# Kernel tuning notes

Hardware: AMD Instinct MI355X
Metric: run time of the kernel (lower is better)

## Reference

```python
import jax, jax.numpy as jnp
import numpy as np

B, L, C, A = 32, 50, 80, 3
IMG = 480.0
STRIDES = (8, 16, 32)
OBJ_SCALE, NOOBJ_SCALE, CLS_SCALE, COORD_SCALE = 5.0, 1.0, 1.0, 1.0
IOU_IGNORE = 0.6


def setup_inputs() -> dict:
    key = jax.random.key(0)
    ks = jax.random.split(key, 8)
    anchors = jnp.array([[0.05, 0.07], [0.12, 0.15], [0.25, 0.30]], jnp.float32)
    preds0 = jax.random.normal(ks[0], (B, 60, 60, A * (5 + C)), jnp.float32)
    preds1 = jax.random.normal(ks[1], (B, 30, 30, A * (5 + C)), jnp.float32)
    preds2 = jax.random.normal(ks[2], (B, 15, 15, A * (5 + C)), jnp.float32)
    cls = jax.random.randint(ks[3], (B, L, 1), 0, C).astype(jnp.float32)
    xy = jax.random.uniform(ks[4], (B, L, 2), minval=0.2, maxval=0.8)
    wh = jax.random.uniform(ks[5], (B, L, 2), minval=0.05, maxval=0.3)
    valid = (jax.random.uniform(ks[6], (B, L, 1)) < 0.6).astype(jnp.float32)
    # gt_labels in loss layout: [cx, cy, w, h, class], padded boxes have w=h=0
    gt_labels = jnp.concatenate([xy, wh * valid, cls], -1)
    return {"preds0": preds0, "preds1": preds1, "preds2": preds2,
            "gt_labels": gt_labels, "anchors": anchors}


def get_detector_mask(gt, anchors_l, H, W):
    # gt: [B,L,5] (cx,cy,w,h,class) normalized; anchors_l in grid units
    Bv, Lv, _ = gt.shape
    Av = anchors_l.shape[0]
    scale = jnp.array([W, H, W, H], jnp.float32)
    box = gt[..., :4] * scale                                  # grid units
    valid = box[..., 2] > 0.0                                  # [B,L]
    j = jnp.clip(jnp.floor(box[..., 0]), 0, W - 1).astype(jnp.int32)
    i = jnp.clip(jnp.floor(box[..., 1]), 0, H - 1).astype(jnp.int32)
    wh = box[..., 2:4]                                         # [B,L,2]
    inter = jnp.prod(jnp.minimum(wh[:, :, None, :], anchors_l[None, None]), -1)
    iou = inter / (jnp.prod(wh, -1)[..., None]
                   + jnp.prod(anchors_l, -1)[None, None] - inter + 1e-9)
    k = jnp.argmax(iou, -1)                                    # best anchor [B,L]
    b = jnp.arange(Bv, dtype=jnp.int32)[:, None]
    N = Bv * H * W * Av
    flat = ((b * H + i) * W + j) * Av + k
    flat = jnp.where(valid, flat, N)                           # invalid -> sentinel
    mask = jnp.zeros(N + 1, jnp.float32).at[flat.reshape(-1)].set(1.0)[:N]
    mask = mask.reshape(Bv, H, W, Av, 1)
    anc = anchors_l[k]                                         # [B,L,2]
    safe_wh = jnp.where(valid[..., None], wh, 1.0)
    adj = jnp.concatenate([
        (box[..., 0] - j.astype(jnp.float32))[..., None],
        (box[..., 1] - i.astype(jnp.float32))[..., None],
        jnp.log(safe_wh / anc),
        gt[..., 4:5]], -1)                                     # [B,L,5]
    mtb = jnp.zeros((N + 1, 5), jnp.float32).at[flat.reshape(-1)].set(
        adj.reshape(-1, 5))[:N].reshape(Bv, H, W, Av, 5)
    return mask, mtb


def yolo_head(feats, anchors_l):
    Bv, H, W, _ = feats.shape
    Av = anchors_l.shape[0]
    f = feats.reshape(Bv, H, W, Av, 5 + C)
    gy, gx = jnp.meshgrid(jnp.arange(H, dtype=jnp.float32),
                          jnp.arange(W, dtype=jnp.float32), indexing='ij')
    grid = jnp.stack([gx, gy], -1)[None, :, :, None, :]        # [1,H,W,1,2]
    conv = jnp.array([W, H], jnp.float32)
    box_xy = jax.nn.sigmoid(f[..., :2])
    box_wh = jnp.exp(f[..., 2:4])
    pred_xy = (box_xy + grid) / conv                           # normalized
    pred_wh = box_wh * anchors_l / conv
    return f, box_xy, pred_xy, pred_wh


def level_loss(f, box_xy, pred_xy, pred_wh, gt, mask, mtb):
    # IoU of every predicted box against every GT box -> ignore mask
    pmin = (pred_xy - pred_wh * 0.5)[..., None, :]             # [B,H,W,A,1,2]
    pmax = (pred_xy + pred_wh * 0.5)[..., None, :]
    tmin = (gt[..., :2] - gt[..., 2:4] * 0.5)[:, None, None, None]  # [B,1,1,1,L,2]
    tmax = (gt[..., :2] + gt[..., 2:4] * 0.5)[:, None, None, None]
    wh_i = jnp.clip(jnp.minimum(pmax, tmax) - jnp.maximum(pmin, tmin), 0.0)
    inter = jnp.prod(wh_i, -1)                                 # [B,H,W,A,L]
    parea = jnp.prod(pred_wh, -1)[..., None]
    tarea = jnp.prod(gt[..., 2:4], -1)[:, None, None, None]
    iou = inter / (parea + tarea - inter + 1e-9)
    best = jnp.max(iou, -1, keepdims=True)                     # [B,H,W,A,1]
    obj_det = (best > IOU_IGNORE).astype(f.dtype)
    pred_conf = jax.nn.sigmoid(f[..., 4:5])
    no_obj_loss = NOOBJ_SCALE * (1.0 - obj_det) * (1.0 - mask) * pred_conf ** 2
    obj_loss = OBJ_SCALE * mask * (1.0 - pred_conf) ** 2
    pred_class = jax.nn.softmax(f[..., 5:], -1)
    onehot = jax.nn.one_hot(mtb[..., 4].astype(jnp.int32), C, dtype=f.dtype)
    cls_loss = CLS_SCALE * mask * (onehot - pred_class) ** 2
    pred_boxes = jnp.concatenate([box_xy, f[..., 2:4]], -1)
    coord_loss = COORD_SCALE * mask * (mtb[..., :4] - pred_boxes) ** 2
    return 0.5 * (jnp.sum(no_obj_loss) + jnp.sum(obj_loss)
                  + jnp.sum(cls_loss) + jnp.sum(coord_loss))


def decode(f, pred_xy, pred_wh):
    Bv = f.shape[0]
    bmin = (pred_xy - pred_wh * 0.5) * IMG
    bmax = (pred_xy + pred_wh * 0.5) * IMG
    boxes = jnp.concatenate([bmin, bmax], -1).reshape(Bv, -1, 4)
    scores = (jax.nn.sigmoid(f[..., 4:5])
              * jax.nn.softmax(f[..., 5:], -1)).reshape(Bv, -1, C)
    return boxes, scores


def reference(preds0, preds1, preds2, gt_labels, anchors):
    loss = jnp.float32(0.0)
    boxes_l, scores_l = [], []
    for preds, stride in zip((preds0, preds1, preds2), STRIDES):
        H = W = int(IMG) // stride
        anc = anchors * (IMG / stride)                         # grid units
        mask, mtb = get_detector_mask(gt_labels, anc, H, W)
        f, box_xy, pred_xy, pred_wh = yolo_head(preds, anc)
        loss = loss + level_loss(f, box_xy, pred_xy, pred_wh, gt_labels, mask, mtb)
        bx, sc = decode(f, pred_xy, pred_wh)
        boxes_l.append(bx)
        scores_l.append(sc)
    boxes = jnp.concatenate(boxes_l, axis=1)
    scores = jnp.concatenate(scores_l, axis=1)
    return loss, boxes, scores
```

## Files before the change

kernel.cpp:

```cpp
#include <hip/hip_runtime.h>
#include <math.h>

#define BB 32
#define LL 50
#define CC 80
#define AA 3
#define IMGF 480.0f
#define ROWS_TOTAL 14175
#define BOX_OFF 1L
#define SCORE_OFF (1L + (long)BB * ROWS_TOTAL * 4)

#define CB0 10800
#define CB1 2700
#define CB2 675

#define CH0 169
#define CH1 43
#define CH2 11
#define BLK0 (BB * CH0)
#define BLK1 (BB * CH1)
#define BLK2 (BB * CH2)
#define NBLK (BLK0 + BLK1 + BLK2)

#define WS_CREC  0
#define WS_NVAL  (BB * LL * 8 * 4)
#define WS_PART  (WS_NVAL + 128)

__global__ __launch_bounds__(64) void setup_kernel(const float* __restrict__ gt,
                                                   const float* __restrict__ anchors,
                                                   char* __restrict__ ws)
{
    int b    = blockIdx.x;
    int lane = threadIdx.x;
    float x = 0.f, y = 0.f, w = 0.f, h = 0.f, cls = 0.f;
    bool valid = false;
    if (lane < LL) {
        const float* g = gt + (b * LL + lane) * 5;
        x = g[0]; y = g[1]; w = g[2]; h = g[3]; cls = g[4];
        valid = (w > 0.0f);
    }
    unsigned long long m = __ballot(valid);
    int pos = (int)__popcll(m & ((1ull << lane) - 1ull));
    if (lane == 0) ((int*)(ws + WS_NVAL))[b] = (int)__popcll(m);
    if (valid) {
        int kpack = 0;
#pragma unroll
        for (int lvl = 0; lvl < 3; ++lvl) {
            float Wf = (lvl == 0) ? 60.f : (lvl == 1) ? 30.f : 15.f;
            float bw = w * Wf, bh = h * Wf;
            float best = -1.0f; int kb = 0;
#pragma unroll
            for (int kk = 0; kk < AA; ++kk) {
                float aw = anchors[kk * 2 + 0] * Wf;
                float ah = anchors[kk * 2 + 1] * Wf;
                float inter = fminf(bw, aw) * fminf(bh, ah);
                float iou = inter / (bw * bh + aw * ah - inter + 1e-9f);
                if (iou > best) { best = iou; kb = kk; }
            }
            kpack |= kb << (2 * lvl);
        }
        float* r = (float*)(ws + WS_CREC) + (b * LL + pos) * 8;
        r[0] = x; r[1] = y; r[2] = w; r[3] = h;
        r[4] = cls; r[5] = (float)kpack; r[6] = 0.6f * (w * h); r[7] = 0.f;
    }
}

__global__ __launch_bounds__(256) void main_kernel(
    const float* __restrict__ preds0,
    const float* __restrict__ preds1,
    const float* __restrict__ preds2,
    const float* __restrict__ anchors,
    const char* __restrict__ wsc,
    float* __restrict__ partials,
    float* __restrict__ out)
{
    const float* crec = (const float*)(wsc + WS_CREC);
    const int*   nval = (const int*)(wsc + WS_NVAL);

    int bid = blockIdx.x;
    const float* preds; int W, cells_b, rowoff, b, chunk, lvl;
    float invW; unsigned Wmagic;
    if (bid < BLK0) {
        lvl = 0; preds = preds0; W = 60; invW = 1.0f / 60.0f; Wmagic = 71582789u;
        cells_b = CB0; rowoff = 0;
        b = bid / CH0; chunk = bid - b * CH0;
    } else if (bid < BLK0 + BLK1) {
        int inner = bid - BLK0;
        lvl = 1; preds = preds1; W = 30; invW = 1.0f / 30.0f; Wmagic = 143165577u;
        cells_b = CB1; rowoff = CB0;
        b = inner / CH1; chunk = inner - b * CH1;
    } else {
        int inner = bid - BLK0 - BLK1;
        lvl = 2; preds = preds2; W = 15; invW = 1.0f / 15.0f; Wmagic = 286331154u;
        cells_b = CB2; rowoff = CB0 + CB1;
        b = inner / CH2; chunk = inner - b * CH2;
    }
    float Wf = (float)W;

    int tid = threadIdx.x;
    int g   = tid >> 2;
    int sub = tid & 3;
    int cell = chunk * 64 + g;
    bool cvalid = cell < cells_b;
    int cc = cvalid ? cell : (cells_b - 1);

    int t1 = cc / 3;
    int a  = cc - t1 * 3;
    int h  = (int)__umulhi((unsigned)t1, Wmagic);
    int w  = t1 - h * W;

    long pbase = ((long)b * cells_b + cc) * 85;
    const float* p = preds + pbase;
    float f0 = p[0], f1 = p[1], f2 = p[2], f3 = p[3], f4 = p[4];

    const float* pc = p + 5 + 4 * sub;
    float4 q0 = *(const float4*)(pc);
    float4 q1 = *(const float4*)(pc + 16);
    float4 q2 = *(const float4*)(pc + 32);
    float4 q3 = *(const float4*)(pc + 48);
    float4 q4 = *(const float4*)(pc + 64);

    int nv = nval[b];

    q0.x = __expf(q0.x); q0.y = __expf(q0.y); q0.z = __expf(q0.z); q0.w = __expf(q0.w);
    q1.x = __expf(q1.x); q1.y = __expf(q1.y); q1.z = __expf(q1.z); q1.w = __expf(q1.w);
    q2.x = __expf(q2.x); q2.y = __expf(q2.y); q2.z = __expf(q2.z); q2.w = __expf(q2.w);
    q3.x = __expf(q3.x); q3.y = __expf(q3.y); q3.z = __expf(q3.z); q3.w = __expf(q3.w);
    q4.x = __expf(q4.x); q4.y = __expf(q4.y); q4.z = __expf(q4.z); q4.w = __expf(q4.w);
    float s = (q0.x + q0.y + q0.z + q0.w) + (q1.x + q1.y + q1.z + q1.w)
            + (q2.x + q2.y + q2.z + q2.w) + (q3.x + q3.y + q3.z + q3.w)
            + (q4.x + q4.y + q4.z + q4.w);
    s += __shfl_xor(s, 1);
    s += __shfl_xor(s, 2);
    float invs = __builtin_amdgcn_rcpf(s);

    float conf = __builtin_amdgcn_rcpf(1.0f + __expf(-f4));
    float bxs  = __builtin_amdgcn_rcpf(1.0f + __expf(-f0));
    float bys  = __builtin_amdgcn_rcpf(1.0f + __expf(-f1));
    float ancw = anchors[2 * a], anch = anchors[2 * a + 1];
    float pw = __expf(f2) * ancw;
    float ph = __expf(f3) * anch;
    float px = (bxs + (float)w) * invW;
    float py = (bys + (float)h) * invW;
    float pminx = px - 0.5f * pw, pmaxx = px + 0.5f * pw;
    float pminy = py - 0.5f * ph, pmaxy = py + 0.5f * ph;
    float pa06 = 0.6f * (pw * ph) + 0.6e-9f;

    const float* cb = crec + b * LL * 8;
    float amax = -1.0f;
    int wtloc = -1;
    for (int t = sub; t < nv; t += 4) {
        const float* r = cb + t * 8;
        float4 rA = *(const float4*)r;
        float4 rB = *(const float4*)(r + 4);
        float tminx = rA.x - 0.5f * rA.z, tmaxx = rA.x + 0.5f * rA.z;
        float tminy = rA.y - 0.5f * rA.w, tmaxy = rA.y + 0.5f * rA.w;
        float ix = fmaxf(fminf(pmaxx, tmaxx) - fmaxf(pminx, tminx), 0.0f);
        float iy = fmaxf(fminf(pmaxy, tmaxy) - fmaxf(pminy, tminy), 0.0f);
        amax = fmaxf(amax, 1.6f * (ix * iy) - (pa06 + rB.z));
        float bxg = rA.x * Wf, byg = rA.y * Wf;
        int jg = min(max((int)floorf(bxg), 0), W - 1);
        int ig = min(max((int)floorf(byg), 0), W - 1);
        int kg = (((int)rB.y) >> (2 * lvl)) & 3;
        int cellt = (ig * W + jg) * 3 + kg;
        if (cellt == cc) wtloc = (t > wtloc) ? t : wtloc;
    }
    unsigned long long bal = __ballot(amax > 0.0f);
    bool objdet = ((bal >> (tid & 60)) & 0xFULL) != 0ULL;

    {
        int o1 = __shfl_xor(wtloc, 1); wtloc = (o1 > wtloc) ? o1 : wtloc;
        int o2 = __shfl_xor(wtloc, 2); wtloc = (o2 > wtloc) ? o2 : wtloc;
    }
    int wt = wtloc;

    float ar0 = 0.f, ar1 = 0.f, ar2 = 0.f, ar3 = 0.f; int label = -1;
    if (wt >= 0) {
        const float* r = cb + wt * 8;
        label = (int)r[4];
        if (sub == 0) {
            float bxg = r[0] * Wf, byg = r[1] * Wf;
            float bwg = r[2] * Wf, bhg = r[3] * Wf;
            int jg = min(max((int)floorf(bxg), 0), W - 1);
            int ig = min(max((int)floorf(byg), 0), W - 1);
            int kg = (((int)r[5]) >> (2 * lvl)) & 3;
            float kaw = anchors[2 * kg + 0] * Wf;
            float kah = anchors[2 * kg + 1] * Wf;
            ar0 = bxg - (float)jg;
            ar1 = byg - (float)ig;
            ar2 = logf(bwg / kaw);
            ar3 = logf(bhg / kah);
        }
    }

    float partial = 0.0f;
    float ci = conf * invs;
    if (cvalid) {
        long rb = (long)b * ROWS_TOTAL + rowoff + cell;
        float* sb = out + SCORE_OFF + rb * CC + 4 * sub;
        float4 o;
        o.x = q0.x * ci; o.y = q0.y * ci; o.z = q0.z * ci; o.w = q0.w * ci; *(float4*)(sb)      = o;
        o.x = q1.x * ci; o.y = q1.y * ci; o.z = q1.z * ci; o.w = q1.w * ci; *(float4*)(sb + 16) = o;
        o.x = q2.x * ci; o.y = q2.y * ci; o.z = q2.z * ci; o.w = q2.w * ci; *(float4*)(sb + 32) = o;
        o.x = q3.x * ci; o.y = q3.y * ci; o.z = q3.z * ci; o.w = q3.w * ci; *(float4*)(sb + 48) = o;
        o.x = q4.x * ci; o.y = q4.y * ci; o.z = q4.z * ci; o.w = q4.w * ci; *(float4*)(sb + 64) = o;
        {
            float comp = (sub == 0) ? pminx : (sub == 1) ? pminy
                       : (sub == 2) ? pmaxx : pmaxy;
            out[BOX_OFF + rb * 4 + sub] = comp * IMGF;
        }

        if (wt >= 0) {
            int c = 4 * sub;
            float d;
            d = ((c +  0) == label ? 1.0f : 0.0f) - q0.x * invs; partial += d * d;
            d = ((c +  1) == label ? 1.0f : 0.0f) - q0.y * invs; partial += d * d;
            d = ((c +  2) == label ? 1.0f : 0.0f) - q0.z * invs; partial += d * d;
            d = ((c +  3) == label ? 1.0f : 0.0f) - q0.w * invs; partial += d * d;
            d = ((c + 16) == label ? 1.0f : 0.0f) - q1.x * invs; partial += d * d;
            d = ((c + 17) == label ? 1.0f : 0.0f) - q1.y * invs; partial += d * d;
            d = ((c + 18) == label ? 1.0f : 0.0f) - q1.z * invs; partial += d * d;
            d = ((c + 19) == label ? 1.0f : 0.0f) - q1.w * invs; partial += d * d;
            d = ((c + 32) == label ? 1.0f : 0.0f) - q2.x * invs; partial += d * d;
            d = ((c + 33) == label ? 1.0f : 0.0f) - q2.y * invs; partial += d * d;
            d = ((c + 34) == label ? 1.0f : 0.0f) - q2.z * invs; partial += d * d;
            d = ((c + 35) == label ? 1.0f : 0.0f) - q2.w * invs; partial += d * d;
            d = ((c + 48) == label ? 1.0f : 0.0f) - q3.x * invs; partial += d * d;
            d = ((c + 49) == label ? 1.0f : 0.0f) - q3.y * invs; partial += d * d;
            d = ((c + 50) == label ? 1.0f : 0.0f) - q3.z * invs; partial += d * d;
            d = ((c + 51) == label ? 1.0f : 0.0f) - q3.w * invs; partial += d * d;
            d = ((c + 64) == label ? 1.0f : 0.0f) - q4.x * invs; partial += d * d;
            d = ((c + 65) == label ? 1.0f : 0.0f) - q4.y * invs; partial += d * d;
            d = ((c + 66) == label ? 1.0f : 0.0f) - q4.z * invs; partial += d * d;
            d = ((c + 67) == label ? 1.0f : 0.0f) - q4.w * invs; partial += d * d;
            if (sub == 0) {
                float c0 = ar0 - bxs, c1 = ar1 - bys;
                float c2 = ar2 - f2,  c3 = ar3 - f3;
                partial += c0 * c0 + c1 * c1 + c2 * c2 + c3 * c3;
                float u = 1.0f - conf;
                partial += 5.0f * u * u;
            }
        } else if (sub == 0) {
            partial += (objdet ? 0.0f : 1.0f) * conf * conf;
        }
    }

    float vsum = partial;
#pragma unroll
    for (int off = 32; off; off >>= 1) vsum += __shfl_xor(vsum, off);
    __shared__ float red[4];
    int wave = tid >> 6;
    if ((tid & 63) == 0) red[wave] = vsum;
    __syncthreads();
    if (tid == 0) partials[bid] = 0.5f * (red[0] + red[1] + red[2] + red[3]);
}

__global__ void reduce_kernel(const float* __restrict__ partials,
                              float* __restrict__ out)
{
    __shared__ float red[4];
    float s = 0.0f;
    for (int i = threadIdx.x; i < NBLK; i += 256) s += partials[i];
#pragma unroll
    for (int off = 32; off; off >>= 1) s += __shfl_xor(s, off);
    int wave = threadIdx.x >> 6;
    if ((threadIdx.x & 63) == 0) red[wave] = s;
    __syncthreads();
    if (threadIdx.x == 0) out[0] = red[0] + red[1] + red[2] + red[3];
}

extern "C" void kernel_launch(void* const* d_in, const int* in_sizes, int n_in,
                              void* d_out, int out_size, void* d_ws, size_t ws_size,
                              hipStream_t stream)
{
    const float* preds0  = (const float*)d_in[0];
    const float* preds1  = (const float*)d_in[1];
    const float* preds2  = (const float*)d_in[2];
    const float* gt      = (const float*)d_in[3];
    const float* anchors = (const float*)d_in[4];
    float* out = (float*)d_out;
    char* ws = (char*)d_ws;

    setup_kernel<<<BB, 64, 0, stream>>>(gt, anchors, ws);
    main_kernel<<<NBLK, 256, 0, stream>>>(preds0, preds1, preds2, anchors,
                                          (const char*)ws,
                                          (float*)(ws + WS_PART), out);
    reduce_kernel<<<1, 256, 0, stream>>>((const float*)(ws + WS_PART), out);
}
```

Measured before the change: 285.8 us.

## Process two cells per thread group and fuse final reduction via last-block atomic

Each block now handles 128 cells instead of 64, with each 4-lane group processing two cells so that the per-box IoU/target loop over ground truths is shared across both cells and block count is halved. The separate reduce kernel is removed and replaced with an atomic counter where the last finishing block sums all partials, saving one kernel launch. This raises register pressure (two sets of 20 class values per thread) which may lower occupancy, and adds an atomic plus fences per block.

```diff
diff --git a/kernel.cpp b/kernel.cpp
--- a/kernel.cpp
+++ b/kernel.cpp
@@ -14,17 +14,18 @@
 #define CB1 2700
 #define CB2 675
 
-#define CH0 169
-#define CH1 43
-#define CH2 11
+#define CH0 85
+#define CH1 22
+#define CH2 6
 #define BLK0 (BB * CH0)
 #define BLK1 (BB * CH1)
 #define BLK2 (BB * CH2)
 #define NBLK (BLK0 + BLK1 + BLK2)
 
 #define WS_CREC  0
-#define WS_NVAL  (BB * LL * 8 * 4)
-#define WS_PART  (WS_NVAL + 128)
+#define WS_NVAL  51200
+#define WS_CNT   51328
+#define WS_PART  51344
 
 __global__ __launch_bounds__(64) void setup_kernel(const float* __restrict__ gt,
                                                    const float* __restrict__ anchors,
@@ -32,6 +33,7 @@
 {
     int b    = blockIdx.x;
     int lane = threadIdx.x;
+    if (b == 0 && lane == 0) *(unsigned*)(ws + WS_CNT) = 0u;
     float x = 0.f, y = 0.f, w = 0.f, h = 0.f, cls = 0.f;
     bool valid = false;
     if (lane < LL) {
@@ -70,12 +72,13 @@
     const float* __restrict__ preds1,
     const float* __restrict__ preds2,
     const float* __restrict__ anchors,
-    const char* __restrict__ wsc,
-    float* __restrict__ partials,
+    char* __restrict__ ws,
     float* __restrict__ out)
 {
-    const float* crec = (const float*)(wsc + WS_CREC);
-    const int*   nval = (const int*)(wsc + WS_NVAL);
+    const float* crec = (const float*)(ws + WS_CREC);
+    const int*   nval = (const int*)(ws + WS_NVAL);
+    float*   partials = (float*)(ws + WS_PART);
+    unsigned*     cnt = (unsigned*)(ws + WS_CNT);
 
     int bid = blockIdx.x;
     const float* preds; int W, cells_b, rowoff, b, chunk, lvl;
@@ -100,148 +103,151 @@
     int tid = threadIdx.x;
     int g   = tid >> 2;
     int sub = tid & 3;
-    int cell = chunk * 64 + g;
-    bool cvalid = cell < cells_b;
-    int cc = cvalid ? cell : (cells_b - 1);
-
-    int t1 = cc / 3;
-    int a  = cc - t1 * 3;
-    int h  = (int)__umulhi((unsigned)t1, Wmagic);
-    int w  = t1 - h * W;
-
-    long pbase = ((long)b * cells_b + cc) * 85;
-    const float* p = preds + pbase;
-    float f0 = p[0], f1 = p[1], f2 = p[2], f3 = p[3], f4 = p[4];
-
-    const float* pc = p + 5 + 4 * sub;
-    float4 q0 = *(const float4*)(pc);
-    float4 q1 = *(const float4*)(pc + 16);
-    float4 q2 = *(const float4*)(pc + 32);
-    float4 q3 = *(const float4*)(pc + 48);
-    float4 q4 = *(const float4*)(pc + 64);
-
+
+    int  cel[2]; bool vld[2]; int ccs[2];
+    float fr[2][5];
+    float4 qv[2][5];
+#pragma unroll
+    for (int e = 0; e < 2; ++e) {
+        int c = chunk * 128 + g + 64 * e;
+        bool v = c < cells_b;
+        int cc = v ? c : cells_b - 1;
+        cel[e] = c; vld[e] = v; ccs[e] = cc;
+        const float* p = preds + ((long)b * cells_b + cc) * 85;
+        fr[e][0] = p[0]; fr[e][1] = p[1]; fr[e][2] = p[2];
+        fr[e][3] = p[3]; fr[e][4] = p[4];
+        const float* pc = p + 5 + 4 * sub;
+        qv[e][0] = *(const float4*)(pc);
+        qv[e][1] = *(const float4*)(pc + 16);
+        qv[e][2] = *(const float4*)(pc + 32);
+        qv[e][3] = *(const float4*)(pc + 48);
+        qv[e][4] = *(const float4*)(pc + 64);
+    }
     int nv = nval[b];
 
-    q0.x = __expf(q0.x); q0.y = __expf(q0.y); q0.z = __expf(q0.z); q0.w = __expf(q0.w);
-    q1.x = __expf(q1.x); q1.y = __expf(q1.y); q1.z = __expf(q1.z); q1.w = __expf(q1.w);
-    q2.x = __expf(q2.x); q2.y = __expf(q2.y); q2.z = __expf(q2.z); q2.w = __expf(q2.w);
-    q3.x = __expf(q3.x); q3.y = __expf(q3.y); q3.z = __expf(q3.z); q3.w = __expf(q3.w);
-    q4.x = __expf(q4.x); q4.y = __expf(q4.y); q4.z = __expf(q4.z); q4.w = __expf(q4.w);
-    float s = (q0.x + q0.y + q0.z + q0.w) + (q1.x + q1.y + q1.z + q1.w)
-            + (q2.x + q2.y + q2.z + q2.w) + (q3.x + q3.y + q3.z + q3.w)
-            + (q4.x + q4.y + q4.z + q4.w);
-    s += __shfl_xor(s, 1);
-    s += __shfl_xor(s, 2);
-    float invs = __builtin_amdgcn_rcpf(s);
-
-    float conf = __builtin_amdgcn_rcpf(1.0f + __expf(-f4));
-    float bxs  = __builtin_amdgcn_rcpf(1.0f + __expf(-f0));
-    float bys  = __builtin_amdgcn_rcpf(1.0f + __expf(-f1));
-    float ancw = anchors[2 * a], anch = anchors[2 * a + 1];
-    float pw = __expf(f2) * ancw;
-    float ph = __expf(f3) * anch;
-    float px = (bxs + (float)w) * invW;
-    float py = (bys + (float)h) * invW;
-    float pminx = px - 0.5f * pw, pmaxx = px + 0.5f * pw;
-    float pminy = py - 0.5f * ph, pmaxy = py + 0.5f * ph;
-    float pa06 = 0.6f * (pw * ph) + 0.6e-9f;
+    float invs[2], conf[2], bxs[2], bys[2];
+    float pminx[2], pmaxx[2], pminy[2], pmaxy[2], pa06[2];
+#pragma unroll
+    for (int e = 0; e < 2; ++e) {
+#pragma unroll
+        for (int k = 0; k < 5; ++k) {
+            qv[e][k].x = __expf(qv[e][k].x);
+            qv[e][k].y = __expf(qv[e][k].y);
+            qv[e][k].z = __expf(qv[e][k].z);
+            qv[e][k].w = __expf(qv[e][k].w);
+        }
+        float s = 0.0f;
+#pragma unroll
+        for (int k = 0; k < 5; ++k)
+            s += qv[e][k].x + qv[e][k].y + qv[e][k].z + qv[e][k].w;
+        s += __shfl_xor(s, 1);
+        s += __shfl_xor(s, 2);
+        invs[e] = __builtin_amdgcn_rcpf(s);
+
+        conf[e] = __builtin_amdgcn_rcpf(1.0f + __expf(-fr[e][4]));
+        bxs[e]  = __builtin_amdgcn_rcpf(1.0f + __expf(-fr[e][0]));
+        bys[e]  = __builtin_amdgcn_rcpf(1.0f + __expf(-fr[e][1]));
+
+        int cc = ccs[e];
+        int t1 = cc / 3;
+        int a  = cc - t1 * 3;
+        int hh = (int)__umulhi((unsigned)t1, Wmagic);
+        int ww = t1 - hh * W;
+        float pw = __expf(fr[e][2]) * anchors[2 * a];
+        float ph = __expf(fr[e][3]) * anchors[2 * a + 1];
+        float px = (bxs[e] + (float)ww) * invW;
+        float py = (bys[e] + (float)hh) * invW;
+        pminx[e] = px - 0.5f * pw; pmaxx[e] = px + 0.5f * pw;
+        pminy[e] = py - 0.5f * ph; pmaxy[e] = py + 0.5f * ph;
+        pa06[e]  = 0.6f * (pw * ph) + 0.6e-9f;
+    }
 
     const float* cb = crec + b * LL * 8;
-    float amax = -1.0f;
-    int wtloc = -1;
+    float amax[2] = {-1.0f, -1.0f};
+    int   wtl[2]  = {-1, -1};
     for (int t = sub; t < nv; t += 4) {
         const float* r = cb + t * 8;
         float4 rA = *(const float4*)r;
         float4 rB = *(const float4*)(r + 4);
         float tminx = rA.x - 0.5f * rA.z, tmaxx = rA.x + 0.5f * rA.z;
         float tminy = rA.y - 0.5f * rA.w, tmaxy = rA.y + 0.5f * rA.w;
-        float ix = fmaxf(fminf(pmaxx, tmaxx) - fmaxf(pminx, tminx), 0.0f);
-        float iy = fmaxf(fminf(pmaxy, tmaxy) - fmaxf(pminy, tminy), 0.0f);
-        amax = fmaxf(amax, 1.6f * (ix * iy) - (pa06 + rB.z));
         float bxg = rA.x * Wf, byg = rA.y * Wf;
         int jg = min(max((int)floorf(bxg), 0), W - 1);
         int ig = min(max((int)floorf(byg), 0), W - 1);
         int kg = (((int)rB.y) >> (2 * lvl)) & 3;
         int cellt = (ig * W + jg) * 3 + kg;
-        if (cellt == cc) wtloc = (t > wtloc) ? t : wtloc;
-    }
-    unsigned long long bal = __ballot(amax > 0.0f);
-    bool objdet = ((bal >> (tid & 60)) & 0xFULL) != 0ULL;
-
-    {
-        int o1 = __shfl_xor(wtloc, 1); wtloc = (o1 > wtloc) ? o1 : wtloc;
-        int o2 = __shfl_xor(wtloc, 2); wtloc = (o2 > wtloc) ? o2 : wtloc;
-    }
-    int wt = wtloc;
-
-    float ar0 = 0.f, ar1 = 0.f, ar2 = 0.f, ar3 = 0.f; int label = -1;
-    if (wt >= 0) {
-        const float* r = cb + wt * 8;
-        label = (int)r[4];
-        if (sub == 0) {
-            float bxg = r[0] * Wf, byg = r[1] * Wf;
-            float bwg = r[2] * Wf, bhg = r[3] * Wf;
-            int jg = min(max((int)floorf(bxg), 0), W - 1);
-            int ig = min(max((int)floorf(byg), 0), W - 1);
-            int kg = (((int)r[5]) >> (2 * lvl)) & 3;
-            float kaw = anchors[2 * kg + 0] * Wf;
-            float kah = anchors[2 * kg + 1] * Wf;
-            ar0 = bxg - (float)jg;
-            ar1 = byg - (float)ig;
-            ar2 = logf(bwg / kaw);
-            ar3 = logf(bhg / kah);
+#pragma unroll
+        for (int e = 0; e < 2; ++e) {
+            float ix = fmaxf(fminf(pmaxx[e], tmaxx) - fmaxf(pminx[e], tminx), 0.0f);
+            float iy = fmaxf(fminf(pmaxy[e], tmaxy) - fmaxf(pminy[e], tminy), 0.0f);
+            amax[e] = fmaxf(amax[e], 1.6f * (ix * iy) - (pa06[e] + rB.z));
+            if (cellt == ccs[e]) wtl[e] = (t > wtl[e]) ? t : wtl[e];
         }
     }
 
     float partial = 0.0f;
-    float ci = conf * invs;
-    if (cvalid) {
-        long rb = (long)b * ROWS_TOTAL + rowoff + cell;
-        float* sb = out + SCORE_OFF + rb * CC + 4 * sub;
-        float4 o;
-        o.x = q0.x * ci; o.y = q0.y * ci; o.z = q0.z * ci; o.w = q0.w * ci; *(float4*)(sb)      = o;
-        o.x = q1.x * ci; o.y = q1.y * ci; o.z = q1.z * ci; o.w = q1.w * ci; *(float4*)(sb + 16) = o;
-        o.x = q2.x * ci; o.y = q2.y * ci; o.z = q2.z * ci; o.w = q2.w * ci; *(float4*)(sb + 32) = o;
-        o.x = q3.x * ci; o.y = q3.y * ci; o.z = q3.z * ci; o.w = q3.w * ci; *(float4*)(sb + 48) = o;
-        o.x = q4.x * ci; o.y = q4.y * ci; o.z = q4.z * ci; o.w = q4.w * ci; *(float4*)(sb + 64) = o;
-        {
-            float comp = (sub == 0) ? pminx : (sub == 1) ? pminy
-                       : (sub == 2) ? pmaxx : pmaxy;
-            out[BOX_OFF + rb * 4 + sub] = comp * IMGF;
-        }
-
+#pragma unroll
+    for (int e = 0; e < 2; ++e) {
+        unsigned long long bal = __ballot(amax[e] > 0.0f);
+        bool objdet = ((bal >> (tid & 60)) & 0xFULL) != 0ULL;
+        int wt = wtl[e];
+        { int o1 = __shfl_xor(wt, 1); wt = (o1 > wt) ? o1 : wt;
+          int o2 = __shfl_xor(wt, 2); wt = (o2 > wt) ? o2 : wt; }
+
+        float ar0 = 0.f, ar1 = 0.f, ar2 = 0.f, ar3 = 0.f; int label = -1;
         if (wt >= 0) {
-            int c = 4 * sub;
-            float d;
-            d = ((c +  0) == label ? 1.0f : 0.0f) - q0.x * invs; partial += d * d;
-            d = ((c +  1) == label ? 1.0f : 0.0f) - q0.y * invs; partial += d * d;
-            d = ((c +  2) == label ? 1.0f : 0.0f) - q0.z * invs; partial += d * d;
-            d = ((c +  3) == label ? 1.0f : 0.0f) - q0.w * invs; partial += d * d;
-            d = ((c + 16) == label ? 1.0f : 0.0f) - q1.x * invs; partial += d * d;
-            d = ((c + 17) == label ? 1.0f : 0.0f) - q1.y * invs; partial += d * d;
-            d = ((c + 18) == label ? 1.0f : 0.0f) - q1.z * invs; partial += d * d;
-            d = ((c + 19) == label ? 1.0f : 0.0f) - q1.w * invs; partial += d * d;
-            d = ((c + 32) == label ? 1.0f : 0.0f) - q2.x * invs; partial += d * d;
-            d = ((c + 33) == label ? 1.0f : 0.0f) - q2.y * invs; partial += d * d;
-            d = ((c + 34) == label ? 1.0f : 0.0f) - q2.z * invs; partial += d * d;
-            d = ((c + 35) == label ? 1.0f : 0.0f) - q2.w * invs; partial += d * d;
-            d = ((c + 48) == label ? 1.0f : 0.0f) - q3.x * invs; partial += d * d;
-            d = ((c + 49) == label ? 1.0f : 0.0f) - q3.y * invs; partial += d * d;
-            d = ((c + 50) == label ? 1.0f : 0.0f) - q3.z * invs; partial += d * d;
-            d = ((c + 51) == label ? 1.0f : 0.0f) - q3.w * invs; partial += d * d;
-            d = ((c + 64) == label ? 1.0f : 0.0f) - q4.x * invs; partial += d * d;
-            d = ((c + 65) == label ? 1.0f : 0.0f) - q4.y * invs; partial += d * d;
-            d = ((c + 66) == label ? 1.0f : 0.0f) - q4.z * invs; partial += d * d;
-            d = ((c + 67) == label ? 1.0f : 0.0f) - q4.w * invs; partial += d * d;
+            const float* r = cb + wt * 8;
+            label = (int)r[4];
             if (sub == 0) {
-                float c0 = ar0 - bxs, c1 = ar1 - bys;
-                float c2 = ar2 - f2,  c3 = ar3 - f3;
-                partial += c0 * c0 + c1 * c1 + c2 * c2 + c3 * c3;
-                float u = 1.0f - conf;
-                partial += 5.0f * u * u;
-            }
-        } else if (sub == 0) {
-            partial += (objdet ? 0.0f : 1.0f) * conf * conf;
+                float bxg = r[0] * Wf, byg = r[1] * Wf;
+                float bwg = r[2] * Wf, bhg = r[3] * Wf;
+                int jg = min(max((int)floorf(bxg), 0), W - 1);
+                int ig = min(max((int)floorf(byg), 0), W - 1);
+                int kg = (((int)r[5]) >> (2 * lvl)) & 3;
+                ar0 = bxg - (float)jg;
+                ar1 = byg - (float)ig;
+                ar2 = logf(bwg / (anchors[2 * kg + 0] * Wf));
+                ar3 = logf(bhg / (anchors[2 * kg + 1] * Wf));
+            }
+        }
+
+        if (vld[e]) {
+            float ci = conf[e] * invs[e];
+            long rb = (long)b * ROWS_TOTAL + rowoff + cel[e];
+            float* sb = out + SCORE_OFF + rb * CC + 4 * sub;
+#pragma unroll
+            for (int k = 0; k < 5; ++k) {
+                float4 o = make_float4(qv[e][k].x * ci, qv[e][k].y * ci,
+                                       qv[e][k].z * ci, qv[e][k].w * ci);
+                *(float4*)(sb + 16 * k) = o;
+            }
+            {
+                float comp = (sub == 0) ? pminx[e] : (sub == 1) ? pminy[e]
+                           : (sub == 2) ? pmaxx[e] : pmaxy[e];
+                out[BOX_OFF + rb * 4 + sub] = comp * IMGF;
+            }
+
+            if (wt >= 0) {
+                int c = 4 * sub;
+                float iv = invs[e];
+#pragma unroll
+                for (int k = 0; k < 5; ++k) {
+                    float d;
+                    d = ((c + 16 * k + 0) == label ? 1.0f : 0.0f) - qv[e][k].x * iv; partial += d * d;
+                    d = ((c + 16 * k + 1) == label ? 1.0f : 0.0f) - qv[e][k].y * iv; partial += d * d;
+                    d = ((c + 16 * k + 2) == label ? 1.0f : 0.0f) - qv[e][k].z * iv; partial += d * d;
+                    d = ((c + 16 * k + 3) == label ? 1.0f : 0.0f) - qv[e][k].w * iv; partial += d * d;
+                }
+                if (sub == 0) {
+                    float c0 = ar0 - bxs[e], c1 = ar1 - bys[e];
+                    float c2 = ar2 - fr[e][2], c3 = ar3 - fr[e][3];
+                    partial += c0 * c0 + c1 * c1 + c2 * c2 + c3 * c3;
+                    float u = 1.0f - conf[e];
+                    partial += 5.0f * u * u;
+                }
+            } else if (sub == 0) {
+                partial += (objdet ? 0.0f : 1.0f) * conf[e] * conf[e];
+            }
         }
     }
 
@@ -249,24 +255,27 @@
 #pragma unroll
     for (int off = 32; off; off >>= 1) vsum += __shfl_xor(vsum, off);
     __shared__ float red[4];
+    __shared__ int lastflag;
     int wave = tid >> 6;
     if ((tid & 63) == 0) red[wave] = vsum;
     __syncthreads();
-    if (tid == 0) partials[bid] = 0.5f * (red[0] + red[1] + red[2] + red[3]);
-}
-
-__global__ void reduce_kernel(const float* __restrict__ partials,
-                              float* __restrict__ out)
-{
-    __shared__ float red[4];
-    float s = 0.0f;
-    for (int i = threadIdx.x; i < NBLK; i += 256) s += partials[i];
-#pragma unroll
-    for (int off = 32; off; off >>= 1) s += __shfl_xor(s, off);
-    int wave = threadIdx.x >> 6;
-    if ((threadIdx.x & 63) == 0) red[wave] = s;
+    if (tid == 0) {
+        partials[bid] = 0.5f * (red[0] + red[1] + red[2] + red[3]);
+        __threadfence();
+        unsigned old = atomicAdd(cnt, 1u);
+        lastflag = (old == (unsigned)(NBLK - 1)) ? 1 : 0;
+    }
     __syncthreads();
-    if (threadIdx.x == 0) out[0] = red[0] + red[1] + red[2] + red[3];
+    if (lastflag) {
+        __threadfence();
+        float s2 = 0.0f;
+        for (int i = tid; i < NBLK; i += 256) s2 += partials[i];
+#pragma unroll
+        for (int off = 32; off; off >>= 1) s2 += __shfl_xor(s2, off);
+        if ((tid & 63) == 0) red[tid >> 6] = s2;
+        __syncthreads();
+        if (tid == 0) out[0] = red[0] + red[1] + red[2] + red[3];
+    }
 }
 
 extern "C" void kernel_launch(void* const* d_in, const int* in_sizes, int n_in,
@@ -283,7 +292,5 @@
 
     setup_kernel<<<BB, 64, 0, stream>>>(gt, anchors, ws);
     main_kernel<<<NBLK, 256, 0, stream>>>(preds0, preds1, preds2, anchors,
-                                          (const char*)ws,
-                                          (float*)(ws + WS_PART), out);
-    reduce_kernel<<<1, 256, 0, stream>>>((const float*)(ws + WS_PART), out);
+                                          ws, out);
 }
```

New measurement: 576.0 us. 102% more time.
